# Kernel optimization log

Measured on AMD Instinct MI355X. Metric: run time of the kernel, lower is better.

The kernel has to match this reference:

```python
import jax, jax.numpy as jnp
import numpy as np

N_GAUSS = 1536
WIDTH, HEIGHT = 160, 128
FX = FY = 146.44        # 2343.024 * (160/2560)
CX, CY = WIDTH / 2.0, HEIGHT / 2.0
EPS2D = 0.3             # 2D covariance dilation (as in prepare_rasterization_coefficients)
NEAR, FAR = 0.01, 1e10


def eval_sh_basis(dirs):
    # real SH basis up to degree 3, 16 components (matches eval_sh_old)
    x, y, z = dirs[..., 0], dirs[..., 1], dirs[..., 2]
    one = jnp.ones_like(x)
    return jnp.stack([
        0.282095 * one,
        -0.488603 * y, 0.488603 * z, -0.488603 * x,
        1.092548 * x * y, -1.092548 * y * z, 0.315392 * (3 * z * z - 1),
        -1.092548 * x * z, 0.546274 * (x * x - y * y),
        -0.590044 * y * (3 * x * x - y * y), 2.890611 * x * y * z,
        -0.457046 * y * (5 * z * z - 1), 0.373176 * z * (5 * z * z - 3),
        -0.457046 * x * (5 * z * z - 1), 1.445306 * z * (x * x - y * y),
        -0.590044 * x * (x * x - 3 * y * y)], axis=-1)


def quat_to_rot(q):
    q = q / jnp.linalg.norm(q, axis=1, keepdims=True)
    w, x, y, z = q[:, 0], q[:, 1], q[:, 2], q[:, 3]
    R = jnp.stack([
        1 - 2 * (y * y + z * z), 2 * (x * y - z * w), 2 * (x * z + y * w),
        2 * (x * y + z * w), 1 - 2 * (x * x + z * z), 2 * (y * z - x * w),
        2 * (x * z - y * w), 2 * (y * z + x * w), 1 - 2 * (x * x + y * y)], axis=-1)
    return R.reshape(-1, 3, 3)


def get_viewmat(c2w):
    # c2w: (B,3,4); flip y/z camera axes then invert (matches torch get_viewmat)
    R = c2w[:, :3, :3] * jnp.array([[[1.0, -1.0, -1.0]]], dtype=c2w.dtype)
    t = c2w[:, :3, 3:4]
    R_inv = jnp.swapaxes(R, 1, 2)
    t_inv = -(R_inv @ t)
    return R_inv[0], t_inv[0, :, 0]


def setup_inputs() -> dict:
    key = jax.random.key(0)
    k0, k1, k2, k3, k4, k5 = jax.random.split(key, 6)
    N = N_GAUSS
    xy = jax.random.normal(k0, (N, 2), dtype=jnp.float32) * 0.5
    # world z negative -> positive camera-frame depth after axis flip
    z = -(1.0 + 4.0 * jax.random.uniform(k1, (N, 1), dtype=jnp.float32))
    means = jnp.concatenate([xy, z], axis=1)
    quats = jax.random.normal(k2, (N, 4), dtype=jnp.float32)
    log_scales = jax.random.normal(k3, (N, 3), dtype=jnp.float32) * 0.3 - 3.0
    opacity_logits = jax.random.normal(k4, (N,), dtype=jnp.float32)
    sh_coeffs = jax.random.normal(k5, (N, 16, 3), dtype=jnp.float32) * 0.3
    camera_to_worlds = jnp.eye(4, dtype=jnp.float32)[None, :3, :]
    return {"means": means, "quats": quats, "log_scales": log_scales,
            "opacity_logits": opacity_logits, "sh_coeffs": sh_coeffs,
            "camera_to_worlds": camera_to_worlds}


def reference(means, quats, log_scales, opacity_logits, sh_coeffs, camera_to_worlds):
    R_w2c, t_w2c = get_viewmat(camera_to_worlds)
    means_cam = means @ R_w2c.T + t_w2c                    # (N,3)
    depth = means_cam[:, 2]
    mask = (depth > NEAR) & (depth < FAR)

    # view-dependent colors from SH (degree 3)
    cam_pos = camera_to_worlds[0, :3, 3]
    dirs = means - cam_pos
    dirs = dirs / jnp.linalg.norm(dirs, axis=1, keepdims=True)
    colors = jnp.maximum(jnp.einsum('nk,nkc->nc', eval_sh_basis(dirs), sh_coeffs) + 0.5, 0.0)

    # 3D covariance -> camera frame -> EWA 2D projection
    Rg = quat_to_rot(quats)                                 # (N,3,3)
    M = Rg * jnp.exp(log_scales)[:, None, :]                # R @ diag(S)
    cov3d = M @ jnp.swapaxes(M, 1, 2)
    cov_cam = jnp.einsum('ij,njk,lk->nil', R_w2c, cov3d, R_w2c)
    tx, ty, tz = means_cam[:, 0], means_cam[:, 1], means_cam[:, 2]
    rz = 1.0 / tz
    zero = jnp.zeros_like(rz)
    J = jnp.stack([jnp.stack([FX * rz, zero, -FX * tx * rz * rz], -1),
                   jnp.stack([zero, FY * rz, -FY * ty * rz * rz], -1)], -2)  # (N,2,3)
    cov2d = jnp.einsum('nij,njk,nlk->nil', J, cov_cam, J)
    a = cov2d[:, 0, 0] + EPS2D
    c = cov2d[:, 1, 1] + EPS2D
    b = cov2d[:, 0, 1]
    det = a * c - b * b
    A, B, C = c / det, -b / det, a / det                    # conic (inverse 2D cov)

    u = FX * tx * rz + CX
    v = FY * ty * rz + CY
    opac = jax.nn.sigmoid(opacity_logits)

    px = jnp.arange(WIDTH, dtype=means.dtype)
    py = jnp.arange(HEIGHT, dtype=means.dtype)
    dx = px[None, None, :] - u[:, None, None]               # (N,1,W)
    dy = py[None, :, None] - v[:, None, None]               # (N,H,1)
    power = (-0.5 * (A[:, None, None] * dx * dx + C[:, None, None] * dy * dy)
             - B[:, None, None] * (dx * dy))                # (N,H,W)
    alpha = jnp.minimum(0.999, opac[:, None, None] * jnp.exp(power))
    alpha = jnp.where(mask[:, None, None], alpha, 0.0)

    # global depth sort (front-to-back alpha compositing)
    order = jnp.argsort(jnp.where(mask, depth, jnp.inf))
    alpha = alpha[order]
    colors = colors[order]
    T = jnp.cumprod(1.0 - alpha, axis=0)
    T_excl = jnp.concatenate([jnp.ones_like(T[:1]), T[:-1]], axis=0)
    w = T_excl * alpha                                      # (N,H,W)
    rgb = jnp.einsum('nhw,nc->hwc', w, colors)              # (H,W,3)
    return rgb
```

## Files before the change

### kernel.cpp

```cpp
#include <hip/hip_runtime.h>
#include <math.h>

#define N_GAUSS 1536
#define WIDTH   160
#define HEIGHT  128
#define NPIX    (WIDTH * HEIGHT)
#define FXC     146.44f
#define FYC     146.44f
#define CXC     80.0f
#define CYC     64.0f
#define EPS2D   0.3f
#define NEARP   0.01f
#define FARP    1e10f
#define L2E     1.4426950408889634f
#define LN2     0.6931471805599453f
#define CULL_E  25.0f

#define PREP_BLOCKS 384
#define PREP_TPB    256
#define SCAN_LEN4   (N_GAUSS / 64 / 4)

#define NWAVE   16
#define RCHUNK  (N_GAUSS / NWAVE)
#define RPIX    64
#define TILE_W  8
#define TILE_H  8
#define TILES_X (WIDTH / TILE_W)
#define TILES_Y (HEIGHT / TILE_H)
#define NTILES  (TILES_X * TILES_Y)
#define RBLOCKS 256

__device__ __forceinline__ float fast_exp2(float x) {
    return __builtin_amdgcn_exp2f(x);
}


__global__ __launch_bounds__(PREP_TPB) void prep_sort_kernel(
    const float* __restrict__ means, const float* __restrict__ quats,
    const float* __restrict__ log_scales, const float* __restrict__ opac_logits,
    const float* __restrict__ sh, const float* __restrict__ c2w,
    float4* __restrict__ bbox, float4* __restrict__ rec)
{
    __shared__ float4 k4_lds[N_GAUSS / 4];
    float* k_lds = (float*)k4_lds;

    float C[12];
#pragma unroll
    for (int k = 0; k < 12; k++) C[k] = c2w[k];
    float R00 =  C[0], R01 =  C[4], R02 =  C[8];
    float R10 = -C[1], R11 = -C[5], R12 = -C[9];
    float R20 = -C[2], R21 = -C[6], R22 = -C[10];
    float cpx = C[3], cpy = C[7], cpz = C[11];
    float t0 = -(R00 * cpx + R01 * cpy + R02 * cpz);
    float t1 = -(R10 * cpx + R11 * cpy + R12 * cpz);
    float t2 = -(R20 * cpx + R21 * cpy + R22 * cpz);

    for (int j = threadIdx.x; j < N_GAUSS; j += PREP_TPB) {
        float mx = means[3 * j], my = means[3 * j + 1], mz = means[3 * j + 2];
        float tzj = R20 * mx + R21 * my + R22 * mz + t2;
        bool m = (tzj > NEARP) && (tzj < FARP);
        k_lds[j] = m ? tzj : INFINITY;
    }
    __syncthreads();

    int i    = blockIdx.x * 4 + (threadIdx.x >> 6);
    int part = threadIdx.x & 63;

    float mx = means[3 * i], my = means[3 * i + 1], mz = means[3 * i + 2];
    float4 qv = ((const float4*)quats)[i];
    float lsx = log_scales[3 * i + 0];
    float lsy = log_scales[3 * i + 1];
    float lsz = log_scales[3 * i + 2];
    float olog = opac_logits[i];
    const float4* sh4 = (const float4*)(sh + i * 48);
    float4 S[12];
#pragma unroll
    for (int k = 0; k < 12; k++) S[k] = sh4[k];
    const float* shf = (const float*)S;

    float tx = R00 * mx + R01 * my + R02 * mz + t0;
    float ty = R10 * mx + R11 * my + R12 * mz + t1;
    float tz = R20 * mx + R21 * my + R22 * mz + t2;
    bool mask = (tz > NEARP) && (tz < FARP);

    float dx = mx - cpx, dy = my - cpy, dz = mz - cpz;
    float rn = rsqrtf(dx * dx + dy * dy + dz * dz);
    float x = dx * rn, y = dy * rn, z = dz * rn;
    float xx = x * x, yy = y * y, zz = z * z;
    float basis[16];
    basis[0]  = 0.282095f;
    basis[1]  = -0.488603f * y;
    basis[2]  = 0.488603f * z;
    basis[3]  = -0.488603f * x;
    basis[4]  = 1.092548f * x * y;
    basis[5]  = -1.092548f * y * z;
    basis[6]  = 0.315392f * (3.f * zz - 1.f);
    basis[7]  = -1.092548f * x * z;
    basis[8]  = 0.546274f * (xx - yy);
    basis[9]  = -0.590044f * y * (3.f * xx - yy);
    basis[10] = 2.890611f * x * y * z;
    basis[11] = -0.457046f * y * (5.f * zz - 1.f);
    basis[12] = 0.373176f * z * (5.f * zz - 3.f);
    basis[13] = -0.457046f * x * (5.f * zz - 1.f);
    basis[14] = 1.445306f * z * (xx - yy);
    basis[15] = -0.590044f * x * (xx - 3.f * yy);
    float cr = 0.f, cg = 0.f, cb = 0.f;
#pragma unroll
    for (int k = 0; k < 16; k++) {
        cr += basis[k] * shf[3 * k + 0];
        cg += basis[k] * shf[3 * k + 1];
        cb += basis[k] * shf[3 * k + 2];
    }
    cr = fmaxf(cr + 0.5f, 0.f);
    cg = fmaxf(cg + 0.5f, 0.f);
    cb = fmaxf(cb + 0.5f, 0.f);

    float qw = qv.x, qx = qv.y, qy = qv.z, qz = qv.w;
    float qn = rsqrtf(qw * qw + qx * qx + qy * qy + qz * qz);
    qw *= qn; qx *= qn; qy *= qn; qz *= qn;
    float sx = expf(lsx);
    float sy = expf(lsy);
    float sz = expf(lsz);
    float M00 = (1.f - 2.f * (qy * qy + qz * qz)) * sx;
    float M01 = (2.f * (qx * qy - qz * qw)) * sy;
    float M02 = (2.f * (qx * qz + qy * qw)) * sz;
    float M10 = (2.f * (qx * qy + qz * qw)) * sx;
    float M11 = (1.f - 2.f * (qx * qx + qz * qz)) * sy;
    float M12 = (2.f * (qy * qz - qx * qw)) * sz;
    float M20 = (2.f * (qx * qz - qy * qw)) * sx;
    float M21 = (2.f * (qy * qz + qx * qw)) * sy;
    float M22 = (1.f - 2.f * (qx * qx + qy * qy)) * sz;
    float V00 = M00 * M00 + M01 * M01 + M02 * M02;
    float V01 = M00 * M10 + M01 * M11 + M02 * M12;
    float V02 = M00 * M20 + M01 * M21 + M02 * M22;
    float V11 = M10 * M10 + M11 * M11 + M12 * M12;
    float V12 = M10 * M20 + M11 * M21 + M12 * M22;
    float V22 = M20 * M20 + M21 * M21 + M22 * M22;

    float T00 = R00 * V00 + R01 * V01 + R02 * V02;
    float T01 = R00 * V01 + R01 * V11 + R02 * V12;
    float T02 = R00 * V02 + R01 * V12 + R02 * V22;
    float T10 = R10 * V00 + R11 * V01 + R12 * V02;
    float T11 = R10 * V01 + R11 * V11 + R12 * V12;
    float T12 = R10 * V02 + R11 * V12 + R12 * V22;
    float T20 = R20 * V00 + R21 * V01 + R22 * V02;
    float T21 = R20 * V01 + R21 * V11 + R22 * V12;
    float T22 = R20 * V02 + R21 * V12 + R22 * V22;
    float cc00 = T00 * R00 + T01 * R01 + T02 * R02;
    float cc01 = T00 * R10 + T01 * R11 + T02 * R12;
    float cc02 = T00 * R20 + T01 * R21 + T02 * R22;
    float cc11 = T10 * R10 + T11 * R11 + T12 * R12;
    float cc12 = T10 * R20 + T11 * R21 + T12 * R22;
    float cc22 = T20 * R20 + T21 * R21 + T22 * R22;

    float rz = 1.f / tz;
    float rz2 = rz * rz;
    float j00 = FXC * rz, j02 = -FXC * tx * rz2;
    float j11 = FYC * rz, j12 = -FYC * ty * rz2;
    float c2d00 = j00 * j00 * cc00 + 2.f * j00 * j02 * cc02 + j02 * j02 * cc22;
    float c2d01 = (j00 * cc01 + j02 * cc12) * j11 + (j00 * cc02 + j02 * cc22) * j12;
    float c2d11 = j11 * j11 * cc11 + 2.f * j11 * j12 * cc12 + j12 * j12 * cc22;

    float a = c2d00 + EPS2D, c = c2d11 + EPS2D, b = c2d01;
    float idet = 1.f / (a * c - b * b);
    float Ac = c * idet, Bc = -b * idet, Cc = a * idet;
    float u = FXC * tx * rz + CXC;
    float v = FYC * ty * rz + CYC;
    float op = 1.f / (1.f + expf(-olog));
    float a2 = -0.5f * L2E * Ac;
    float b2 = -L2E * Bc;
    float c2 = -0.5f * L2E * Cc;
    float o2 = log2f(op);

    float Qmax = fmaxf(0.f, 2.f * LN2 * (CULL_E + o2));
    float rx = sqrtf(Qmax * a);
    float ry = sqrtf(Qmax * c);

    if (!mask) {
        u = 1e30f; v = 1e30f; rx = 0.f; ry = 0.f;
        a2 = 0.f; b2 = 0.f; c2 = 0.f; o2 = -INFINITY;
    }

    float ki = k_lds[i];
    int rank = 0;
    int base4 = part * SCAN_LEN4;
#pragma unroll
    for (int jj = 0; jj < SCAN_LEN4; jj++) {
        int j4 = base4 + jj;
        float4 kk = k4_lds[j4];
        int j = 4 * j4;
        rank += (kk.x < ki) || (kk.x == ki && (j + 0) < i);
        rank += (kk.y < ki) || (kk.y == ki && (j + 1) < i);
        rank += (kk.z < ki) || (kk.z == ki && (j + 2) < i);
        rank += (kk.w < ki) || (kk.w == ki && (j + 3) < i);
    }
    rank += __shfl_xor(rank, 1);
    rank += __shfl_xor(rank, 2);
    rank += __shfl_xor(rank, 4);
    rank += __shfl_xor(rank, 8);
    rank += __shfl_xor(rank, 16);
    rank += __shfl_xor(rank, 32);

    if (part == 0) {
        bbox[rank]        = make_float4(u, v, rx, ry);
        rec[3 * rank + 0] = make_float4(u, v, a2, b2);
        rec[3 * rank + 1] = make_float4(c2, o2, cr, cg);
        rec[3 * rank + 2] = make_float4(cb, 0.f, 0.f, 0.f);
    }
}

__global__ __launch_bounds__(1024) void raster_kernel(
    const float4* __restrict__ bbox, const float4* __restrict__ rec,
    float* __restrict__ out)
{
    __shared__ float4 part_lds[NWAVE * RPIX];

    int wave = __builtin_amdgcn_readfirstlane(threadIdx.x >> 6);
    int lane = threadIdx.x & 63;
    int g0 = wave * RCHUNK;

    int ntile = (blockIdx.x < NTILES - RBLOCKS) ? 2 : 1;
    for (int ti = 0; ti < ntile; ti++) {
        int tile = (ti == 0) ? blockIdx.x : (RBLOCKS + blockIdx.x);
        int tx0 = (tile % TILES_X) * TILE_W;
        int ty0 = (tile / TILES_X) * TILE_H;
        float px = (float)(tx0 + (lane & 7));
        float py = (float)(ty0 + (lane >> 3));
        float tcx = (float)tx0 + 3.5f;
        float tcy = (float)ty0 + 3.5f;

        float4 bb0 = bbox[g0 + lane];
        float4 bb1 = bbox[g0 + 64 + (lane & 31)];
        bool ok0 = (fabsf(tcx - bb0.x) <= bb0.z + 3.5f) &&
                   (fabsf(tcy - bb0.y) <= bb0.w + 3.5f);
        bool ok1 = (lane < 32) &&
                   (fabsf(tcx - bb1.x) <= bb1.z + 3.5f) &&
                   (fabsf(tcy - bb1.y) <= bb1.w + 3.5f);
        unsigned long long m0 = __ballot(ok0);
        unsigned long long m1 = __ballot(ok1);

        float T = 1.f, cr = 0.f, cg = 0.f, cb = 0.f;
#pragma unroll
        for (int bseg = 0; bseg < 2; bseg++) {
            unsigned long long m = bseg ? m1 : m0;
            int gbase = g0 + (bseg ? 64 : 0);
            while (m) {
                int bl = __ffsll(m) - 1;
                m &= m - 1;
                int g = gbase + bl;
                float4 f0 = rec[3 * g + 0];
                float4 f1 = rec[3 * g + 1];
                float4 f2 = rec[3 * g + 2];
                float dx = px - f0.x;
                float dy = py - f0.y;
                float t  = f0.z * dx;
                t = fmaf(f0.w, dy, t);
                float q  = f1.x * dy;
                float pw = fmaf(t, dx, f1.y);
                pw = fmaf(q, dy, pw);
                float alpha = fminf(0.999f, fast_exp2(pw));
                float w = T * alpha;
                cr = fmaf(w, f1.z, cr);
                cg = fmaf(w, f1.w, cg);
                cb = fmaf(w, f2.x, cb);
                T -= w;
            }
        }
        part_lds[wave * RPIX + lane] = make_float4(cr, cg, cb, T);
        __syncthreads();

        if (threadIdx.x < RPIX) {
            int l = threadIdx.x;
            int p = (ty0 + (l >> 3)) * WIDTH + tx0 + (l & 7);
            float Tt = 1.f, r = 0.f, g = 0.f, b = 0.f;
#pragma unroll
            for (int c = 0; c < NWAVE; c++) {
                float4 qq = part_lds[c * RPIX + l];
                r = fmaf(Tt, qq.x, r);
                g = fmaf(Tt, qq.y, g);
                b = fmaf(Tt, qq.z, b);
                Tt *= qq.w;
            }
            out[3 * p + 0] = r;
            out[3 * p + 1] = g;
            out[3 * p + 2] = b;
        }
        if (ti + 1 < ntile) __syncthreads();
    }
}

extern "C" void kernel_launch(void* const* d_in, const int* in_sizes, int n_in,
                              void* d_out, int out_size, void* d_ws, size_t ws_size,
                              hipStream_t stream) {
    const float* means       = (const float*)d_in[0];
    const float* quats       = (const float*)d_in[1];
    const float* log_scales  = (const float*)d_in[2];
    const float* opac_logits = (const float*)d_in[3];
    const float* sh          = (const float*)d_in[4];
    const float* c2w         = (const float*)d_in[5];

    float* ws = (float*)d_ws;
    float4* bbox = (float4*)ws;
    float4* rec  = (float4*)(ws + N_GAUSS * 4);

    prep_sort_kernel<<<PREP_BLOCKS, PREP_TPB, 0, stream>>>(
        means, quats, log_scales, opac_logits, sh, c2w, bbox, rec);
    raster_kernel<<<RBLOCKS, NWAVE * 64, 0, stream>>>(
        bbox, rec, (float*)d_out);
}
```

Before: 79.01 us.

## Fuse preprocessing, per-tile culling and sort into single raster kernel

```diff
diff --git a/kernel.cpp b/kernel.cpp
--- a/kernel.cpp
+++ b/kernel.cpp
@@ -4,7 +4,6 @@
 #define N_GAUSS 1536
 #define WIDTH   160
 #define HEIGHT  128
-#define NPIX    (WIDTH * HEIGHT)
 #define FXC     146.44f
 #define FYC     146.44f
 #define CXC     80.0f
@@ -16,13 +15,8 @@
 #define LN2     0.6931471805599453f
 #define CULL_E  25.0f
 
-#define PREP_BLOCKS 384
-#define PREP_TPB    256
-#define SCAN_LEN4   (N_GAUSS / 64 / 4)
-
+#define TPB     1024
 #define NWAVE   16
-#define RCHUNK  (N_GAUSS / NWAVE)
-#define RPIX    64
 #define TILE_W  8
 #define TILE_H  8
 #define TILES_X (WIDTH / TILE_W)
@@ -30,19 +24,35 @@
 #define NTILES  (TILES_X * TILES_Y)
 #define RBLOCKS 256
 
+#define OFF_REC   0
+#define OFF_KEY   73728
+#define OFF_RNK   86016
+#define OFF_ORD   92160
+#define OFF_PART  98304
+#define OFF_CNT   114688
+#define SMEM_SZ   114704
+
 __device__ __forceinline__ float fast_exp2(float x) {
     return __builtin_amdgcn_exp2f(x);
 }
 
-
-__global__ __launch_bounds__(PREP_TPB) void prep_sort_kernel(
+__global__ __launch_bounds__(TPB) void fused_kernel(
     const float* __restrict__ means, const float* __restrict__ quats,
     const float* __restrict__ log_scales, const float* __restrict__ opac_logits,
     const float* __restrict__ sh, const float* __restrict__ c2w,
-    float4* __restrict__ bbox, float4* __restrict__ rec)
+    float* __restrict__ out)
 {
-    __shared__ float4 k4_lds[N_GAUSS / 4];
-    float* k_lds = (float*)k4_lds;
+    extern __shared__ unsigned char smem[];
+    float4*             srec  = (float4*)(smem + OFF_REC);
+    unsigned long long* key64 = (unsigned long long*)(smem + OFF_KEY);
+    int*                rnk   = (int*)(smem + OFF_RNK);
+    int*                ord   = (int*)(smem + OFF_ORD);
+    float4*             part  = (float4*)(smem + OFF_PART);
+    int*                cntp  = (int*)(smem + OFF_CNT);
+
+    int tid  = threadIdx.x;
+    int wave = __builtin_amdgcn_readfirstlane(tid >> 6);
+    int lane = tid & 63;
 
     float C[12];
 #pragma unroll
@@ -55,173 +65,9 @@
     float t1 = -(R10 * cpx + R11 * cpy + R12 * cpz);
     float t2 = -(R20 * cpx + R21 * cpy + R22 * cpz);
 
-    for (int j = threadIdx.x; j < N_GAUSS; j += PREP_TPB) {
-        float mx = means[3 * j], my = means[3 * j + 1], mz = means[3 * j + 2];
-        float tzj = R20 * mx + R21 * my + R22 * mz + t2;
-        bool m = (tzj > NEARP) && (tzj < FARP);
-        k_lds[j] = m ? tzj : INFINITY;
-    }
-    __syncthreads();
-
-    int i    = blockIdx.x * 4 + (threadIdx.x >> 6);
-    int part = threadIdx.x & 63;
-
-    float mx = means[3 * i], my = means[3 * i + 1], mz = means[3 * i + 2];
-    float4 qv = ((const float4*)quats)[i];
-    float lsx = log_scales[3 * i + 0];
-    float lsy = log_scales[3 * i + 1];
-    float lsz = log_scales[3 * i + 2];
-    float olog = opac_logits[i];
-    const float4* sh4 = (const float4*)(sh + i * 48);
-    float4 S[12];
-#pragma unroll
-    for (int k = 0; k < 12; k++) S[k] = sh4[k];
-    const float* shf = (const float*)S;
-
-    float tx = R00 * mx + R01 * my + R02 * mz + t0;
-    float ty = R10 * mx + R11 * my + R12 * mz + t1;
-    float tz = R20 * mx + R21 * my + R22 * mz + t2;
-    bool mask = (tz > NEARP) && (tz < FARP);
-
-    float dx = mx - cpx, dy = my - cpy, dz = mz - cpz;
-    float rn = rsqrtf(dx * dx + dy * dy + dz * dz);
-    float x = dx * rn, y = dy * rn, z = dz * rn;
-    float xx = x * x, yy = y * y, zz = z * z;
-    float basis[16];
-    basis[0]  = 0.282095f;
-    basis[1]  = -0.488603f * y;
-    basis[2]  = 0.488603f * z;
-    basis[3]  = -0.488603f * x;
-    basis[4]  = 1.092548f * x * y;
-    basis[5]  = -1.092548f * y * z;
-    basis[6]  = 0.315392f * (3.f * zz - 1.f);
-    basis[7]  = -1.092548f * x * z;
-    basis[8]  = 0.546274f * (xx - yy);
-    basis[9]  = -0.590044f * y * (3.f * xx - yy);
-    basis[10] = 2.890611f * x * y * z;
-    basis[11] = -0.457046f * y * (5.f * zz - 1.f);
-    basis[12] = 0.373176f * z * (5.f * zz - 3.f);
-    basis[13] = -0.457046f * x * (5.f * zz - 1.f);
-    basis[14] = 1.445306f * z * (xx - yy);
-    basis[15] = -0.590044f * x * (xx - 3.f * yy);
-    float cr = 0.f, cg = 0.f, cb = 0.f;
-#pragma unroll
-    for (int k = 0; k < 16; k++) {
-        cr += basis[k] * shf[3 * k + 0];
-        cg += basis[k] * shf[3 * k + 1];
-        cb += basis[k] * shf[3 * k + 2];
-    }
-    cr = fmaxf(cr + 0.5f, 0.f);
-    cg = fmaxf(cg + 0.5f, 0.f);
-    cb = fmaxf(cb + 0.5f, 0.f);
-
-    float qw = qv.x, qx = qv.y, qy = qv.z, qz = qv.w;
-    float qn = rsqrtf(qw * qw + qx * qx + qy * qy + qz * qz);
-    qw *= qn; qx *= qn; qy *= qn; qz *= qn;
-    float sx = expf(lsx);
-    float sy = expf(lsy);
-    float sz = expf(lsz);
-    float M00 = (1.f - 2.f * (qy * qy + qz * qz)) * sx;
-    float M01 = (2.f * (qx * qy - qz * qw)) * sy;
-    float M02 = (2.f * (qx * qz + qy * qw)) * sz;
-    float M10 = (2.f * (qx * qy + qz * qw)) * sx;
-    float M11 = (1.f - 2.f * (qx * qx + qz * qz)) * sy;
-    float M12 = (2.f * (qy * qz - qx * qw)) * sz;
-    float M20 = (2.f * (qx * qz - qy * qw)) * sx;
-    float M21 = (2.f * (qy * qz + qx * qw)) * sy;
-    float M22 = (1.f - 2.f * (qx * qx + qy * qy)) * sz;
-    float V00 = M00 * M00 + M01 * M01 + M02 * M02;
-    float V01 = M00 * M10 + M01 * M11 + M02 * M12;
-    float V02 = M00 * M20 + M01 * M21 + M02 * M22;
-    float V11 = M10 * M10 + M11 * M11 + M12 * M12;
-    float V12 = M10 * M20 + M11 * M21 + M12 * M22;
-    float V22 = M20 * M20 + M21 * M21 + M22 * M22;
-
-    float T00 = R00 * V00 + R01 * V01 + R02 * V02;
-    float T01 = R00 * V01 + R01 * V11 + R02 * V12;
-    float T02 = R00 * V02 + R01 * V12 + R02 * V22;
-    float T10 = R10 * V00 + R11 * V01 + R12 * V02;
-    float T11 = R10 * V01 + R11 * V11 + R12 * V12;
-    float T12 = R10 * V02 + R11 * V12 + R12 * V22;
-    float T20 = R20 * V00 + R21 * V01 + R22 * V02;
-    float T21 = R20 * V01 + R21 * V11 + R22 * V12;
-    float T22 = R20 * V02 + R21 * V12 + R22 * V22;
-    float cc00 = T00 * R00 + T01 * R01 + T02 * R02;
-    float cc01 = T00 * R10 + T01 * R11 + T02 * R12;
-    float cc02 = T00 * R20 + T01 * R21 + T02 * R22;
-    float cc11 = T10 * R10 + T11 * R11 + T12 * R12;
-    float cc12 = T10 * R20 + T11 * R21 + T12 * R22;
-    float cc22 = T20 * R20 + T21 * R21 + T22 * R22;
-
-    float rz = 1.f / tz;
-    float rz2 = rz * rz;
-    float j00 = FXC * rz, j02 = -FXC * tx * rz2;
-    float j11 = FYC * rz, j12 = -FYC * ty * rz2;
-    float c2d00 = j00 * j00 * cc00 + 2.f * j00 * j02 * cc02 + j02 * j02 * cc22;
-    float c2d01 = (j00 * cc01 + j02 * cc12) * j11 + (j00 * cc02 + j02 * cc22) * j12;
-    float c2d11 = j11 * j11 * cc11 + 2.f * j11 * j12 * cc12 + j12 * j12 * cc22;
-
-    float a = c2d00 + EPS2D, c = c2d11 + EPS2D, b = c2d01;
-    float idet = 1.f / (a * c - b * b);
-    float Ac = c * idet, Bc = -b * idet, Cc = a * idet;
-    float u = FXC * tx * rz + CXC;
-    float v = FYC * ty * rz + CYC;
-    float op = 1.f / (1.f + expf(-olog));
-    float a2 = -0.5f * L2E * Ac;
-    float b2 = -L2E * Bc;
-    float c2 = -0.5f * L2E * Cc;
-    float o2 = log2f(op);
-
-    float Qmax = fmaxf(0.f, 2.f * LN2 * (CULL_E + o2));
-    float rx = sqrtf(Qmax * a);
-    float ry = sqrtf(Qmax * c);
-
-    if (!mask) {
-        u = 1e30f; v = 1e30f; rx = 0.f; ry = 0.f;
-        a2 = 0.f; b2 = 0.f; c2 = 0.f; o2 = -INFINITY;
-    }
-
-    float ki = k_lds[i];
-    int rank = 0;
-    int base4 = part * SCAN_LEN4;
-#pragma unroll
-    for (int jj = 0; jj < SCAN_LEN4; jj++) {
-        int j4 = base4 + jj;
-        float4 kk = k4_lds[j4];
-        int j = 4 * j4;
-        rank += (kk.x < ki) || (kk.x == ki && (j + 0) < i);
-        rank += (kk.y < ki) || (kk.y == ki && (j + 1) < i);
-        rank += (kk.z < ki) || (kk.z == ki && (j + 2) < i);
-        rank += (kk.w < ki) || (kk.w == ki && (j + 3) < i);
-    }
-    rank += __shfl_xor(rank, 1);
-    rank += __shfl_xor(rank, 2);
-    rank += __shfl_xor(rank, 4);
-    rank += __shfl_xor(rank, 8);
-    rank += __shfl_xor(rank, 16);
-    rank += __shfl_xor(rank, 32);
-
-    if (part == 0) {
-        bbox[rank]        = make_float4(u, v, rx, ry);
-        rec[3 * rank + 0] = make_float4(u, v, a2, b2);
-        rec[3 * rank + 1] = make_float4(c2, o2, cr, cg);
-        rec[3 * rank + 2] = make_float4(cb, 0.f, 0.f, 0.f);
-    }
-}
-
-__global__ __launch_bounds__(1024) void raster_kernel(
-    const float4* __restrict__ bbox, const float4* __restrict__ rec,
-    float* __restrict__ out)
-{
-    __shared__ float4 part_lds[NWAVE * RPIX];
-
-    int wave = __builtin_amdgcn_readfirstlane(threadIdx.x >> 6);
-    int lane = threadIdx.x & 63;
-    int g0 = wave * RCHUNK;
-
     int ntile = (blockIdx.x < NTILES - RBLOCKS) ? 2 : 1;
     for (int ti = 0; ti < ntile; ti++) {
-        int tile = (ti == 0) ? blockIdx.x : (RBLOCKS + blockIdx.x);
+        int tile = (ti == 0) ? (int)blockIdx.x : (RBLOCKS + (int)blockIdx.x);
         int tx0 = (tile % TILES_X) * TILE_W;
         int ty0 = (tile / TILES_X) * TILE_H;
         float px = (float)(tx0 + (lane & 7));
@@ -229,57 +75,208 @@
         float tcx = (float)tx0 + 3.5f;
         float tcy = (float)ty0 + 3.5f;
 
-        float4 bb0 = bbox[g0 + lane];
-        float4 bb1 = bbox[g0 + 64 + (lane & 31)];
-        bool ok0 = (fabsf(tcx - bb0.x) <= bb0.z + 3.5f) &&
-                   (fabsf(tcy - bb0.y) <= bb0.w + 3.5f);
-        bool ok1 = (lane < 32) &&
-                   (fabsf(tcx - bb1.x) <= bb1.z + 3.5f) &&
-                   (fabsf(tcy - bb1.y) <= bb1.w + 3.5f);
-        unsigned long long m0 = __ballot(ok0);
-        unsigned long long m1 = __ballot(ok1);
-
-        float T = 1.f, cr = 0.f, cg = 0.f, cb = 0.f;
-#pragma unroll
-        for (int bseg = 0; bseg < 2; bseg++) {
-            unsigned long long m = bseg ? m1 : m0;
-            int gbase = g0 + (bseg ? 64 : 0);
-            while (m) {
-                int bl = __ffsll(m) - 1;
-                m &= m - 1;
-                int g = gbase + bl;
-                float4 f0 = rec[3 * g + 0];
-                float4 f1 = rec[3 * g + 1];
-                float4 f2 = rec[3 * g + 2];
-                float dx = px - f0.x;
-                float dy = py - f0.y;
-                float t  = f0.z * dx;
-                t = fmaf(f0.w, dy, t);
-                float q  = f1.x * dy;
-                float pw = fmaf(t, dx, f1.y);
-                pw = fmaf(q, dy, pw);
-                float alpha = fminf(0.999f, fast_exp2(pw));
-                float w = T * alpha;
-                cr = fmaf(w, f1.z, cr);
-                cg = fmaf(w, f1.w, cg);
-                cb = fmaf(w, f2.x, cb);
-                T -= w;
+        if (tid == 0) *cntp = 0;
+        rnk[tid] = 0;
+        if (tid < N_GAUSS - TPB) rnk[TPB + tid] = 0;
+        __syncthreads();
+
+        int slotA = -1, slotB = -1;
+#pragma unroll
+        for (int rep = 0; rep < 2; rep++) {
+            int g = tid + (rep << 10);
+            if (g < N_GAUSS) {
+                float mx = means[3 * g], my = means[3 * g + 1], mz = means[3 * g + 2];
+                float4 qv = ((const float4*)quats)[g];
+                float lsx = log_scales[3 * g + 0];
+                float lsy = log_scales[3 * g + 1];
+                float lsz = log_scales[3 * g + 2];
+                float olog = opac_logits[g];
+
+                float tx = R00 * mx + R01 * my + R02 * mz + t0;
+                float ty = R10 * mx + R11 * my + R12 * mz + t1;
+                float tz = R20 * mx + R21 * my + R22 * mz + t2;
+                bool mask = (tz > NEARP) && (tz < FARP);
+
+                float qw = qv.x, qx = qv.y, qy = qv.z, qz = qv.w;
+                float qn = rsqrtf(qw * qw + qx * qx + qy * qy + qz * qz);
+                qw *= qn; qx *= qn; qy *= qn; qz *= qn;
+                float sx = expf(lsx);
+                float sy = expf(lsy);
+                float sz = expf(lsz);
+                float M00 = (1.f - 2.f * (qy * qy + qz * qz)) * sx;
+                float M01 = (2.f * (qx * qy - qz * qw)) * sy;
+                float M02 = (2.f * (qx * qz + qy * qw)) * sz;
+                float M10 = (2.f * (qx * qy + qz * qw)) * sx;
+                float M11 = (1.f - 2.f * (qx * qx + qz * qz)) * sy;
+                float M12 = (2.f * (qy * qz - qx * qw)) * sz;
+                float M20 = (2.f * (qx * qz - qy * qw)) * sx;
+                float M21 = (2.f * (qy * qz + qx * qw)) * sy;
+                float M22 = (1.f - 2.f * (qx * qx + qy * qy)) * sz;
+                float V00 = M00 * M00 + M01 * M01 + M02 * M02;
+                float V01 = M00 * M10 + M01 * M11 + M02 * M12;
+                float V02 = M00 * M20 + M01 * M21 + M02 * M22;
+                float V11 = M10 * M10 + M11 * M11 + M12 * M12;
+                float V12 = M10 * M20 + M11 * M21 + M12 * M22;
+                float V22 = M20 * M20 + M21 * M21 + M22 * M22;
+
+                float T00 = R00 * V00 + R01 * V01 + R02 * V02;
+                float T01 = R00 * V01 + R01 * V11 + R02 * V12;
+                float T02 = R00 * V02 + R01 * V12 + R02 * V22;
+                float T10 = R10 * V00 + R11 * V01 + R12 * V02;
+                float T11 = R10 * V01 + R11 * V11 + R12 * V12;
+                float T12 = R10 * V02 + R11 * V12 + R12 * V22;
+                float T20 = R20 * V00 + R21 * V01 + R22 * V02;
+                float T21 = R20 * V01 + R21 * V11 + R22 * V12;
+                float T22 = R20 * V02 + R21 * V12 + R22 * V22;
+                float cc00 = T00 * R00 + T01 * R01 + T02 * R02;
+                float cc01 = T00 * R10 + T01 * R11 + T02 * R12;
+                float cc02 = T00 * R20 + T01 * R21 + T02 * R22;
+                float cc11 = T10 * R10 + T11 * R11 + T12 * R12;
+                float cc12 = T10 * R20 + T11 * R21 + T12 * R22;
+                float cc22 = T20 * R20 + T21 * R21 + T22 * R22;
+
+                float rz = 1.f / tz;
+                float rz2 = rz * rz;
+                float j00 = FXC * rz, j02 = -FXC * tx * rz2;
+                float j11 = FYC * rz, j12 = -FYC * ty * rz2;
+                float c2d00 = j00 * j00 * cc00 + 2.f * j00 * j02 * cc02 + j02 * j02 * cc22;
+                float c2d01 = (j00 * cc01 + j02 * cc12) * j11 + (j00 * cc02 + j02 * cc22) * j12;
+                float c2d11 = j11 * j11 * cc11 + 2.f * j11 * j12 * cc12 + j12 * j12 * cc22;
+
+                float a = c2d00 + EPS2D, c = c2d11 + EPS2D, b = c2d01;
+                float idet = 1.f / (a * c - b * b);
+                float Ac = c * idet, Bc = -b * idet, Cc = a * idet;
+                float u = FXC * tx * rz + CXC;
+                float v = FYC * ty * rz + CYC;
+                float op = 1.f / (1.f + expf(-olog));
+                float a2 = -0.5f * L2E * Ac;
+                float b2 = -L2E * Bc;
+                float c2 = -0.5f * L2E * Cc;
+                float o2 = log2f(op);
+
+                float Qmax = fmaxf(0.f, 2.f * LN2 * (CULL_E + o2));
+                float rx = sqrtf(Qmax * a);
+                float ry = sqrtf(Qmax * c);
+                bool hit = mask && (fabsf(tcx - u) <= rx + 3.5f)
+                                && (fabsf(tcy - v) <= ry + 3.5f);
+
+                unsigned long long hm = __ballot(hit);
+                int base = 0;
+                if (lane == 0) {
+                    int nw = __popcll(hm);
+                    if (nw) base = atomicAdd(cntp, nw);
+                }
+                base = __shfl(base, 0);
+                if (hit) {
+                    int slot = base + __popcll(hm & ((1ull << lane) - 1ull));
+                    srec[3 * slot + 0] = make_float4(u, v, a2, b2);
+                    srec[3 * slot + 1] = make_float4(c2, o2, 0.f, 0.f);
+                    key64[slot] = (((unsigned long long)__float_as_uint(tz)) << 32)
+                                  | (unsigned long long)(unsigned)g;
+                    if (rep == 0) slotA = slot; else slotB = slot;
+                }
             }
         }
-        part_lds[wave * RPIX + lane] = make_float4(cr, cg, cb, T);
-        __syncthreads();
-
-        if (threadIdx.x < RPIX) {
-            int l = threadIdx.x;
-            int p = (ty0 + (l >> 3)) * WIDTH + tx0 + (l & 7);
+        __syncthreads();
+        int cnt = __builtin_amdgcn_readfirstlane(*cntp);
+
+        for (int s = tid; s < cnt; s += TPB) {
+            int g = (int)(key64[s] & 0xffffffffull);
+            float mx = means[3 * g], my = means[3 * g + 1], mz = means[3 * g + 2];
+            float dxv = mx - cpx, dyv = my - cpy, dzv = mz - cpz;
+            float rn = rsqrtf(dxv * dxv + dyv * dyv + dzv * dzv);
+            float x = dxv * rn, y = dyv * rn, z = dzv * rn;
+            float xx = x * x, yy = y * y, zz = z * z;
+            float basis[16];
+            basis[0]  = 0.282095f;
+            basis[1]  = -0.488603f * y;
+            basis[2]  = 0.488603f * z;
+            basis[3]  = -0.488603f * x;
+            basis[4]  = 1.092548f * x * y;
+            basis[5]  = -1.092548f * y * z;
+            basis[6]  = 0.315392f * (3.f * zz - 1.f);
+            basis[7]  = -1.092548f * x * z;
+            basis[8]  = 0.546274f * (xx - yy);
+            basis[9]  = -0.590044f * y * (3.f * xx - yy);
+            basis[10] = 2.890611f * x * y * z;
+            basis[11] = -0.457046f * y * (5.f * zz - 1.f);
+            basis[12] = 0.373176f * z * (5.f * zz - 3.f);
+            basis[13] = -0.457046f * x * (5.f * zz - 1.f);
+            basis[14] = 1.445306f * z * (xx - yy);
+            basis[15] = -0.590044f * x * (xx - 3.f * yy);
+            const float4* sh4 = (const float4*)(sh + g * 48);
+            float4 S[12];
+#pragma unroll
+            for (int k = 0; k < 12; k++) S[k] = sh4[k];
+            const float* shf = (const float*)S;
+            float cr = 0.f, cg = 0.f, cb = 0.f;
+#pragma unroll
+            for (int k = 0; k < 16; k++) {
+                cr += basis[k] * shf[3 * k + 0];
+                cg += basis[k] * shf[3 * k + 1];
+                cb += basis[k] * shf[3 * k + 2];
+            }
+            cr = fmaxf(cr + 0.5f, 0.f);
+            cg = fmaxf(cg + 0.5f, 0.f);
+            cb = fmaxf(cb + 0.5f, 0.f);
+            float* rp = (float*)&srec[3 * s + 1];
+            rp[2] = cr;
+            rp[3] = cg;
+            ((float*)&srec[3 * s + 2])[0] = cb;
+        }
+        {
+            int seg = tid & 3;
+            for (int s = (tid >> 2); s < cnt; s += (TPB >> 2)) {
+                unsigned long long ks = key64[s];
+                int tA = (cnt * seg) >> 2;
+                int tB = (cnt * (seg + 1)) >> 2;
+                int partial = 0;
+                for (int t = tA; t < tB; t++)
+                    partial += (key64[t] < ks) ? 1 : 0;
+                if (partial) atomicAdd(&rnk[s], partial);
+            }
+        }
+        __syncthreads();
+        if (slotA >= 0) ord[rnk[slotA]] = slotA;
+        if (slotB >= 0) ord[rnk[slotB]] = slotB;
+        __syncthreads();
+
+        int L = (cnt + NWAVE - 1) >> 4;
+        int r0 = wave * L;
+        int r1 = r0 + L; if (r1 > cnt) r1 = cnt;
+        float T = 1.f, ar = 0.f, ag = 0.f, ab = 0.f;
+        for (int r = r0; r < r1; r++) {
+            int slot = ord[r];
+            float4 f0 = srec[3 * slot + 0];
+            float4 f1 = srec[3 * slot + 1];
+            float4 f2 = srec[3 * slot + 2];
+            float ddx = px - f0.x;
+            float ddy = py - f0.y;
+            float tt = f0.z * ddx;
+            tt = fmaf(f0.w, ddy, tt);
+            float qq = f1.x * ddy;
+            float pw = fmaf(tt, ddx, f1.y);
+            pw = fmaf(qq, ddy, pw);
+            float alpha = fminf(0.999f, fast_exp2(pw));
+            float w = T * alpha;
+            ar = fmaf(w, f1.z, ar);
+            ag = fmaf(w, f1.w, ag);
+            ab = fmaf(w, f2.x, ab);
+            T -= w;
+        }
+        part[wave * 64 + lane] = make_float4(ar, ag, ab, T);
+        __syncthreads();
+
+        if (tid < 64) {
+            int p = (ty0 + (tid >> 3)) * WIDTH + tx0 + (tid & 7);
             float Tt = 1.f, r = 0.f, g = 0.f, b = 0.f;
 #pragma unroll
-            for (int c = 0; c < NWAVE; c++) {
-                float4 qq = part_lds[c * RPIX + l];
-                r = fmaf(Tt, qq.x, r);
-                g = fmaf(Tt, qq.y, g);
-                b = fmaf(Tt, qq.z, b);
-                Tt *= qq.w;
+            for (int cchunk = 0; cchunk < NWAVE; cchunk++) {
+                float4 q4 = part[cchunk * 64 + tid];
+                r = fmaf(Tt, q4.x, r);
+                g = fmaf(Tt, q4.y, g);
+                b = fmaf(Tt, q4.z, b);
+                Tt *= q4.w;
             }
             out[3 * p + 0] = r;
             out[3 * p + 1] = g;
@@ -299,12 +296,6 @@
     const float* sh          = (const float*)d_in[4];
     const float* c2w         = (const float*)d_in[5];
 
-    float* ws = (float*)d_ws;
-    float4* bbox = (float4*)ws;
-    float4* rec  = (float4*)(ws + N_GAUSS * 4);
-
-    prep_sort_kernel<<<PREP_BLOCKS, PREP_TPB, 0, stream>>>(
-        means, quats, log_scales, opac_logits, sh, c2w, bbox, rec);
-    raster_kernel<<<RBLOCKS, NWAVE * 64, 0, stream>>>(
-        bbox, rec, (float*)d_out);
+    fused_kernel<<<RBLOCKS, TPB, SMEM_SZ, stream>>>(
+        means, quats, log_scales, opac_logits, sh, c2w, (float*)d_out);
 }
```

After: 85.33 us. 8.0% more time.
